# Kernel optimization log

Hardware: AMD Instinct MI355X
Metric: run time of the kernel (lower is better)

Reference implementation:

```python
import jax, jax.numpy as jnp
import numpy as np

N_NODES = 100000
N_EDGES = 1600000
IN_CH = 128
OUT_CH = 128


def setup_inputs() -> dict:
    key = jax.random.key(0)
    k1, k2, k3 = jax.random.split(key, 3)
    x = jax.random.normal(k1, (N_NODES, IN_CH), dtype=jnp.float32)
    edge_index = jax.random.randint(k2, (2, N_EDGES), 0, N_NODES, dtype=jnp.int64)
    # glorot-like init for the linear weight, stored as [in, out]
    W = jax.random.normal(k3, (IN_CH, OUT_CH), dtype=jnp.float32) * (2.0 / (IN_CH + OUT_CH)) ** 0.5
    bias = jnp.zeros((OUT_CH,), dtype=jnp.float32)
    return {"x": x, "edge_index": edge_index, "W": W, "bias": bias}


def reference(x, edge_index, W, bias):
    N = x.shape[0]
    # linear transform (bias-free, matches Linear(in, out, bias=False))
    h = x @ W  # [N, out]

    # add self loops (improved=False -> fill_value = 1.0)
    loop = jnp.arange(N, dtype=edge_index.dtype)
    src = jnp.concatenate([edge_index[0], loop])
    dst = jnp.concatenate([edge_index[1], loop])
    ew = jnp.ones(src.shape[0], dtype=h.dtype)  # edge_weight None -> ones

    # symmetric GCN normalization: deg from dst, norm = d^-1/2[src] * w * d^-1/2[dst]
    deg = jax.ops.segment_sum(ew, dst, num_segments=N)
    deg_inv_sqrt = jnp.where(deg > 0, jax.lax.rsqrt(deg), 0.0)
    w = deg_inv_sqrt[src] * ew * deg_inv_sqrt[dst]

    # spmm aggregation: out[dst] += w * h[src]
    out = jax.ops.segment_sum(h[src] * w[:, None], dst, num_segments=N)
    return out + bias
```

## Files before the change

kernel.cpp:

```cpp
#include <hip/hip_runtime.h>
#include <hip/hip_bf16.h>

constexpr int kNodes = 100000;
constexpr int kEdges = 1600000;
constexpr int kCh    = 128;
constexpr int kCap   = 32;
constexpr int kOvfCap = 4096;
constexpr int kLOvf  = 512;
constexpr int kBinShift = 8;
constexpr int kBinSize  = 1 << kBinShift;
constexpr int kBins  = (kNodes + kBinSize - 1) >> kBinShift;
constexpr int kABlocks = 128;
constexpr int kChunkCap = 64;
constexpr int kGemmBlocks = (kNodes + 127) / 128;
constexpr int kAggBlocks = (kNodes + 63) / 64;

typedef __attribute__((ext_vector_type(8))) short short8;
typedef __attribute__((ext_vector_type(4))) float floatx4;
typedef __attribute__((ext_vector_type(4))) int   intx4;


__global__ __launch_bounds__(512) void k_fused(const float* __restrict__ x,
                                               const float* __restrict__ W,
                                               const int* __restrict__ srcArr,
                                               const int* __restrict__ dstArr,
                                               unsigned* __restrict__ segs,
                                               int* __restrict__ segCnt,
                                               int* __restrict__ ovfCnt,
                                               int* __restrict__ ovfD,
                                               int* __restrict__ ovfS,
                                               __hip_bfloat16* __restrict__ hs) {
  if (blockIdx.x < kABlocks) {
    __shared__ int lcnt[kBins];
    for (int i = threadIdx.x; i < kBins; i += 512) lcnt[i] = 0;
    __syncthreads();
    const intx4* d4 = (const intx4*)dstArr;
    const intx4* s4 = (const intx4*)srcArr;
    unsigned* myseg = segs + (long)blockIdx.x * kBins * kChunkCap;
    for (int i = blockIdx.x * 512 + (int)threadIdx.x; i < kEdges / 4; i += kABlocks * 512) {
      intx4 dv = __builtin_nontemporal_load(d4 + i);
      intx4 sv = __builtin_nontemporal_load(s4 + i);
      #pragma unroll
      for (int k = 0; k < 4; k++) {
        int d = dv[k], s = sv[k];
        int bin = d >> kBinShift;
        int pos = atomicAdd(&lcnt[bin], 1);
        if (pos < kChunkCap) {
          myseg[bin * kChunkCap + pos] = ((unsigned)(d & (kBinSize - 1)) << 17) | (unsigned)s;
        } else {
          int o = atomicAdd(ovfCnt, 1);
          if (o < kOvfCap) { ovfD[o] = d; ovfS[o] = s; }
        }
      }
    }
    __syncthreads();
    for (int i = threadIdx.x; i < kBins; i += 512) {
      int c = lcnt[i];
      segCnt[blockIdx.x * kBins + i] = c < kChunkCap ? c : kChunkCap;
    }
    return;
  }

  __shared__ short8 Bf[2048];
  for (int e = threadIdx.x; e < 2048; e += 512) {
    int lane = e & 63, c = (e >> 6) & 3, tt = e >> 8;
    int quad = lane >> 4, mcol = lane & 15;
    short8 v;
    #pragma unroll
    for (int j = 0; j < 8; j++) {
      __hip_bfloat16 h = __float2bfloat16(W[(c * 32 + quad * 8 + j) * kCh + tt * 16 + mcol]);
      v[j] = *(short*)&h;
    }
    Bf[e] = v;
  }
  __syncthreads();

  int wave = threadIdx.x >> 6;
  int lane = threadIdx.x & 63;
  int quad = lane >> 4;
  int mcol = lane & 15;
  int gb = blockIdx.x - kABlocks;
  long rowBase = ((long)gb * 8 + wave) * 16;
  if (rowBase >= kNodes) return;

  long arow = rowBase + mcol;
  if (arow >= kNodes) arow = kNodes - 1;
  const float* xp = x + arow * kCh;
  short8 afrag[4];
  #pragma unroll
  for (int c = 0; c < 4; c++) {
    const floatx4* p = (const floatx4*)(xp + c * 32 + quad * 8);
    floatx4 v0 = __builtin_nontemporal_load(p);
    floatx4 v1 = __builtin_nontemporal_load(p + 1);
    #pragma unroll
    for (int j = 0; j < 4; j++) {
      __hip_bfloat16 h0 = __float2bfloat16(v0[j]);
      __hip_bfloat16 h1 = __float2bfloat16(v1[j]);
      afrag[c][j]     = *(short*)&h0;
      afrag[c][j + 4] = *(short*)&h1;
    }
  }

  #pragma unroll
  for (int t = 0; t < 8; t++) {
    floatx4 acc = {0.f, 0.f, 0.f, 0.f};
    #pragma unroll
    for (int c = 0; c < 4; c++) {
      short8 b = Bf[(t * 4 + c) * 64 + lane];
      acc = __builtin_amdgcn_mfma_f32_16x16x32_bf16(afrag[c], b, acc, 0, 0, 0);
    }
    #pragma unroll
    for (int i = 0; i < 4; i++) {
      long r = rowBase + quad * 4 + i;
      if (r < kNodes) {
        __hip_bfloat16 h = __float2bfloat16(acc[i]);
        __builtin_nontemporal_store(*(short*)&h, (short*)hs + r * kCh + t * 16 + mcol);
      }
    }
  }
}


__global__ __launch_bounds__(256) void k_dinv(const unsigned* __restrict__ segs,
                                              const int* __restrict__ segCnt,
                                              const int* __restrict__ ovfCnt,
                                              const int* __restrict__ ovfD,
                                              float* __restrict__ dinv) {
  __shared__ int lsn[kABlocks];
  __shared__ int hist[kBinSize];
  int bin = blockIdx.x;
  for (int i = threadIdx.x; i < kABlocks; i += 256) lsn[i] = segCnt[i * kBins + bin];
  for (int i = threadIdx.x; i < kBinSize; i += 256) hist[i] = 0;
  __syncthreads();

  for (int slot = threadIdx.x; slot < kABlocks * kChunkCap; slot += 256) {
    int blk = slot >> 6, pos = slot & (kChunkCap - 1);
    if (pos < lsn[blk]) {
      unsigned e = segs[((long)blk * kBins + bin) * kChunkCap + pos];
      atomicAdd(&hist[e >> 17], 1);
    }
  }
  int n = *ovfCnt; if (n > kOvfCap) n = kOvfCap;
  for (int i = threadIdx.x; i < n; i += 256) {
    int d = ovfD[i];
    if ((d >> kBinShift) == bin) atomicAdd(&hist[d & (kBinSize - 1)], 1);
  }
  __syncthreads();
  int base = bin << kBinShift;
  for (int i = threadIdx.x; i < kBinSize; i += 256) {
    int node = base + i;
    if (node < kNodes) dinv[node] = rsqrtf((float)(hist[i] + 1));
  }
}


__global__ __launch_bounds__(512) void k_agg(const unsigned* __restrict__ segs,
                                             const int* __restrict__ segCnt,
                                             const int* __restrict__ ovfCnt,
                                             const int* __restrict__ ovfD,
                                             const int* __restrict__ ovfS,
                                             const float* __restrict__ dinv,
                                             const __hip_bfloat16* __restrict__ hs,
                                             const float* __restrict__ bias,
                                             float* __restrict__ out) {
  __shared__ int lsn[kABlocks];
  __shared__ int lcnt[64];
  __shared__ __align__(16) int lbkt[64][kCap];
  __shared__ unsigned lovf[kLOvf];
  __shared__ int lovfn;

  int base = blockIdx.x * 64;
  int bin  = base >> kBinShift;
  int q    = (base >> 6) & 3;

  for (int i = threadIdx.x; i < kABlocks; i += 512) lsn[i] = segCnt[i * kBins + bin];
  for (int i = threadIdx.x; i < 64; i += 512) lcnt[i] = 0;
  if (threadIdx.x == 0) lovfn = 0;
  __syncthreads();

  for (int slot = threadIdx.x; slot < kABlocks * kChunkCap; slot += 512) {
    int blk = slot >> 6, pos = slot & (kChunkCap - 1);
    if (pos < lsn[blk]) {
      unsigned e = segs[((long)blk * kBins + bin) * kChunkCap + pos];
      int r = (int)(e >> 17) - q * 64;
      if ((unsigned)r < 64u) {
        int p = atomicAdd(&lcnt[r], 1);
        if (p < kCap) lbkt[r][p] = (int)(e & 0x1ffff);
        else { int o = atomicAdd(&lovfn, 1); if (o < kLOvf) lovf[o] = ((unsigned)r << 17) | (e & 0x1ffff); }
      }
    }
  }
  {
    int n = *ovfCnt; if (n > kOvfCap) n = kOvfCap;
    for (int i = threadIdx.x; i < n; i += 512) {
      int d = ovfD[i];
      if ((d >> 6) == blockIdx.x) {
        int r = d & 63;
        int p = atomicAdd(&lcnt[r], 1);
        if (p < kCap) lbkt[r][p] = ovfS[i];
        else { int o = atomicAdd(&lovfn, 1); if (o < kLOvf) lovf[o] = ((unsigned)r << 17) | (unsigned)ovfS[i]; }
      }
    }
  }
  __syncthreads();

  int wave = threadIdx.x >> 6;
  int lane = threadIdx.x & 63;
  const __hip_bfloat162* hbase = (const __hip_bfloat162*)hs;
  int novf = lovfn; if (novf > kLOvf) novf = kLOvf;

  for (int t = 0; t < 8; t++) {
    int r = wave * 8 + t;
    int node = base + r;
    if (node >= kNodes) break;

    float dd = dinv[node];
    float2 sf = __bfloat1622float2(hbase[(long)node * (kCh / 2) + lane]);
    float acc0 = dd * sf.x;
    float acc1 = dd * sf.y;

    int c = lcnt[r]; if (c > kCap) c = kCap;
    int j = 0;
    for (; j + 7 < c; j += 8) {
      int s[8];
      #pragma unroll
      for (int u = 0; u < 8; u++) s[u] = lbkt[r][j + u];
      float dv[8];
      #pragma unroll
      for (int u = 0; u < 8; u++) dv[u] = dinv[s[u]];
      __hip_bfloat162 v[8];
      #pragma unroll
      for (int u = 0; u < 8; u++) v[u] = hbase[(long)s[u] * (kCh / 2) + lane];
      #pragma unroll
      for (int u = 0; u < 8; u++) {
        float2 f = __bfloat1622float2(v[u]);
        acc0 = fmaf(dv[u], f.x, acc0);
        acc1 = fmaf(dv[u], f.y, acc1);
      }
    }
    for (; j < c; ++j) {
      int s = lbkt[r][j];
      float dv = dinv[s];
      float2 f = __bfloat1622float2(hbase[(long)s * (kCh / 2) + lane]);
      acc0 = fmaf(dv, f.x, acc0);
      acc1 = fmaf(dv, f.y, acc1);
    }
    for (int i = 0; i < novf; i++) {
      if ((int)(lovf[i] >> 17) == r) {
        int s = (int)(lovf[i] & 0x1ffff);
        float2 f = __bfloat1622float2(hbase[(long)s * (kCh / 2) + lane]);
        acc0 = fmaf(dinv[s], f.x, acc0);
        acc1 = fmaf(dinv[s], f.y, acc1);
      }
    }

    float2 b = ((const float2*)bias)[lane];
    float2 o;
    o.x = dd * acc0 + b.x;
    o.y = dd * acc1 + b.y;
    ((float2*)(out + (long)node * kCh))[lane] = o;
  }
}


extern "C" void kernel_launch(void* const* d_in, const int* in_sizes, int n_in,
                              void* d_out, int out_size, void* d_ws, size_t ws_size,
                              hipStream_t stream) {
  const float* x    = (const float*)d_in[0];
  const int*   ei   = (const int*)d_in[1];
  const float* W    = (const float*)d_in[2];
  const float* bias = (const float*)d_in[3];
  float* out = (float*)d_out;

  const int* srcArr = ei;
  const int* dstArr = ei + kEdges;

  char* ws = (char*)d_ws;
  size_t off = 0;
  __hip_bfloat16* hs = (__hip_bfloat16*)(ws + off); off += (size_t)kNodes * kCh * 2;
  unsigned* segs = (unsigned*)(ws + off); off += (size_t)kABlocks * kBins * kChunkCap * 4;
  float* dinv    = (float*)   (ws + off); off += (size_t)kNodes * 4;
  int*   segCnt  = (int*)     (ws + off); off += (size_t)kABlocks * kBins * 4;
  int*   ovfCnt  = (int*)     (ws + off); off += 64;
  int*   ovfD    = (int*)     (ws + off); off += (size_t)kOvfCap * 4;
  int*   ovfS    = (int*)     (ws + off); off += (size_t)kOvfCap * 4;

  (void)hipMemsetAsync(ovfCnt, 0, 64, stream);

  k_fused<<<kABlocks + kGemmBlocks, 512, 0, stream>>>(x, W, srcArr, dstArr,
                                                      segs, segCnt, ovfCnt, ovfD, ovfS, hs);

  k_dinv<<<kBins, 256, 0, stream>>>(segs, segCnt, ovfCnt, ovfD, dinv);

  k_agg<<<kAggBlocks, 512, 0, stream>>>(segs, segCnt, ovfCnt, ovfD, ovfS,
                                        dinv, hs, bias, out);
}
```

Baseline: 240.8 us.

## Shrink dst bins to 128 nodes and replace global overflow with per-block spill lists

Bins shrink from 256 to 128 nodes with 32-slot chunks per partition block. The aggregation kernel now handles a whole bin per block, so it no longer scans 256-node bins four times and discards three quarters of the entries. The global atomic overflow list and its memset are replaced by per-block shared-memory spill counters with small per-block spill arrays, and output stores become nontemporal. The risk is that the smaller chunk and spill capacities may silently drop edges on dense bins. With random dst indices, a partition block sees about 16 edges per bin, so 32 slots are usually enough.

```diff
diff --git a/kernel.cpp b/kernel.cpp
--- a/kernel.cpp
+++ b/kernel.cpp
@@ -5,19 +5,19 @@
 constexpr int kEdges = 1600000;
 constexpr int kCh    = 128;
 constexpr int kCap   = 32;
-constexpr int kOvfCap = 4096;
-constexpr int kLOvf  = 512;
-constexpr int kBinShift = 8;
+constexpr int kLOvf  = 256;
+constexpr int kBinShift = 7;
 constexpr int kBinSize  = 1 << kBinShift;
 constexpr int kBins  = (kNodes + kBinSize - 1) >> kBinShift;
 constexpr int kABlocks = 128;
-constexpr int kChunkCap = 64;
+constexpr int kChunkCap = 32;
+constexpr int kSpillCap = 64;
 constexpr int kGemmBlocks = (kNodes + 127) / 128;
-constexpr int kAggBlocks = (kNodes + 63) / 64;
 
 typedef __attribute__((ext_vector_type(8))) short short8;
 typedef __attribute__((ext_vector_type(4))) float floatx4;
 typedef __attribute__((ext_vector_type(4))) int   intx4;
+typedef __attribute__((ext_vector_type(2))) float floatx2;
 
 
 __global__ __launch_bounds__(512) void k_fused(const float* __restrict__ x,
@@ -26,13 +26,15 @@
                                                const int* __restrict__ dstArr,
                                                unsigned* __restrict__ segs,
                                                int* __restrict__ segCnt,
-                                               int* __restrict__ ovfCnt,
-                                               int* __restrict__ ovfD,
-                                               int* __restrict__ ovfS,
+                                               int* __restrict__ spillCnt,
+                                               int* __restrict__ spillD,
+                                               int* __restrict__ spillS,
                                                __hip_bfloat16* __restrict__ hs) {
   if (blockIdx.x < kABlocks) {
     __shared__ int lcnt[kBins];
+    __shared__ int lspilln;
     for (int i = threadIdx.x; i < kBins; i += 512) lcnt[i] = 0;
+    if (threadIdx.x == 0) lspilln = 0;
     __syncthreads();
     const intx4* d4 = (const intx4*)dstArr;
     const intx4* s4 = (const intx4*)srcArr;
@@ -46,10 +48,13 @@
         int bin = d >> kBinShift;
         int pos = atomicAdd(&lcnt[bin], 1);
         if (pos < kChunkCap) {
-          myseg[bin * kChunkCap + pos] = ((unsigned)(d & (kBinSize - 1)) << 17) | (unsigned)s;
+          myseg[(bin << 5) + pos] = ((unsigned)(d & (kBinSize - 1)) << 17) | (unsigned)s;
         } else {
-          int o = atomicAdd(ovfCnt, 1);
-          if (o < kOvfCap) { ovfD[o] = d; ovfS[o] = s; }
+          int o = atomicAdd(&lspilln, 1);
+          if (o < kSpillCap) {
+            spillD[blockIdx.x * kSpillCap + o] = d;
+            spillS[blockIdx.x * kSpillCap + o] = s;
+          }
         }
       }
     }
@@ -57,6 +62,10 @@
     for (int i = threadIdx.x; i < kBins; i += 512) {
       int c = lcnt[i];
       segCnt[blockIdx.x * kBins + i] = c < kChunkCap ? c : kChunkCap;
+    }
+    if (threadIdx.x == 0) {
+      int n = lspilln;
+      spillCnt[blockIdx.x] = n < kSpillCap ? n : kSpillCap;
     }
     return;
   }
@@ -123,27 +132,33 @@
 
 __global__ __launch_bounds__(256) void k_dinv(const unsigned* __restrict__ segs,
                                               const int* __restrict__ segCnt,
-                                              const int* __restrict__ ovfCnt,
-                                              const int* __restrict__ ovfD,
+                                              const int* __restrict__ spillCnt,
+                                              const int* __restrict__ spillD,
                                               float* __restrict__ dinv) {
   __shared__ int lsn[kABlocks];
+  __shared__ int lsp[kABlocks];
   __shared__ int hist[kBinSize];
   int bin = blockIdx.x;
-  for (int i = threadIdx.x; i < kABlocks; i += 256) lsn[i] = segCnt[i * kBins + bin];
+  for (int i = threadIdx.x; i < kABlocks; i += 256) {
+    lsn[i] = segCnt[i * kBins + bin];
+    lsp[i] = spillCnt[i];
+  }
   for (int i = threadIdx.x; i < kBinSize; i += 256) hist[i] = 0;
   __syncthreads();
 
   for (int slot = threadIdx.x; slot < kABlocks * kChunkCap; slot += 256) {
-    int blk = slot >> 6, pos = slot & (kChunkCap - 1);
+    int blk = slot >> 5, pos = slot & 31;
     if (pos < lsn[blk]) {
       unsigned e = segs[((long)blk * kBins + bin) * kChunkCap + pos];
       atomicAdd(&hist[e >> 17], 1);
     }
   }
-  int n = *ovfCnt; if (n > kOvfCap) n = kOvfCap;
-  for (int i = threadIdx.x; i < n; i += 256) {
-    int d = ovfD[i];
-    if ((d >> kBinShift) == bin) atomicAdd(&hist[d & (kBinSize - 1)], 1);
+  for (int i = threadIdx.x; i < kABlocks * kSpillCap; i += 256) {
+    int blk = i >> 6, o = i & 63;
+    if (o < lsp[blk]) {
+      int d = spillD[blk * kSpillCap + o];
+      if ((d >> kBinShift) == bin) atomicAdd(&hist[d & (kBinSize - 1)], 1);
+    }
   }
   __syncthreads();
   int base = bin << kBinShift;
@@ -156,49 +171,51 @@
 
 __global__ __launch_bounds__(512) void k_agg(const unsigned* __restrict__ segs,
                                              const int* __restrict__ segCnt,
-                                             const int* __restrict__ ovfCnt,
-                                             const int* __restrict__ ovfD,
-                                             const int* __restrict__ ovfS,
+                                             const int* __restrict__ spillCnt,
+                                             const int* __restrict__ spillD,
+                                             const int* __restrict__ spillS,
                                              const float* __restrict__ dinv,
                                              const __hip_bfloat16* __restrict__ hs,
                                              const float* __restrict__ bias,
                                              float* __restrict__ out) {
   __shared__ int lsn[kABlocks];
-  __shared__ int lcnt[64];
-  __shared__ __align__(16) int lbkt[64][kCap];
+  __shared__ int lsp[kABlocks];
+  __shared__ int lcnt[kBinSize];
+  __shared__ __align__(16) int lbkt[kBinSize][kCap];
   __shared__ unsigned lovf[kLOvf];
   __shared__ int lovfn;
 
-  int base = blockIdx.x * 64;
-  int bin  = base >> kBinShift;
-  int q    = (base >> 6) & 3;
-
-  for (int i = threadIdx.x; i < kABlocks; i += 512) lsn[i] = segCnt[i * kBins + bin];
-  for (int i = threadIdx.x; i < 64; i += 512) lcnt[i] = 0;
+  int bin  = blockIdx.x;
+  int base = bin << kBinShift;
+
+  for (int i = threadIdx.x; i < kABlocks; i += 512) {
+    lsn[i] = segCnt[i * kBins + bin];
+    lsp[i] = spillCnt[i];
+  }
+  for (int i = threadIdx.x; i < kBinSize; i += 512) lcnt[i] = 0;
   if (threadIdx.x == 0) lovfn = 0;
   __syncthreads();
 
   for (int slot = threadIdx.x; slot < kABlocks * kChunkCap; slot += 512) {
-    int blk = slot >> 6, pos = slot & (kChunkCap - 1);
+    int blk = slot >> 5, pos = slot & 31;
     if (pos < lsn[blk]) {
       unsigned e = segs[((long)blk * kBins + bin) * kChunkCap + pos];
-      int r = (int)(e >> 17) - q * 64;
-      if ((unsigned)r < 64u) {
+      int r = (int)(e >> 17);
+      int p = atomicAdd(&lcnt[r], 1);
+      if (p < kCap) lbkt[r][p] = (int)(e & 0x1ffff);
+      else { int o = atomicAdd(&lovfn, 1); if (o < kLOvf) lovf[o] = ((unsigned)r << 17) | (e & 0x1ffff); }
+    }
+  }
+  for (int i = threadIdx.x; i < kABlocks * kSpillCap; i += 512) {
+    int blk = i >> 6, o = i & 63;
+    if (o < lsp[blk]) {
+      int d = spillD[blk * kSpillCap + o];
+      if ((d >> kBinShift) == bin) {
+        int r = d & (kBinSize - 1);
+        int s = spillS[blk * kSpillCap + o];
         int p = atomicAdd(&lcnt[r], 1);
-        if (p < kCap) lbkt[r][p] = (int)(e & 0x1ffff);
-        else { int o = atomicAdd(&lovfn, 1); if (o < kLOvf) lovf[o] = ((unsigned)r << 17) | (e & 0x1ffff); }
-      }
-    }
-  }
-  {
-    int n = *ovfCnt; if (n > kOvfCap) n = kOvfCap;
-    for (int i = threadIdx.x; i < n; i += 512) {
-      int d = ovfD[i];
-      if ((d >> 6) == blockIdx.x) {
-        int r = d & 63;
-        int p = atomicAdd(&lcnt[r], 1);
-        if (p < kCap) lbkt[r][p] = ovfS[i];
-        else { int o = atomicAdd(&lovfn, 1); if (o < kLOvf) lovf[o] = ((unsigned)r << 17) | (unsigned)ovfS[i]; }
+        if (p < kCap) lbkt[r][p] = s;
+        else { int o2 = atomicAdd(&lovfn, 1); if (o2 < kLOvf) lovf[o2] = ((unsigned)r << 17) | (unsigned)s; }
       }
     }
   }
@@ -209,10 +226,10 @@
   const __hip_bfloat162* hbase = (const __hip_bfloat162*)hs;
   int novf = lovfn; if (novf > kLOvf) novf = kLOvf;
 
-  for (int t = 0; t < 8; t++) {
-    int r = wave * 8 + t;
+  for (int t = 0; t < 16; t++) {
+    int r = wave * 16 + t;
     int node = base + r;
-    if (node >= kNodes) break;
+    if (node >= kNodes) continue;
 
     float dd = dinv[node];
     float2 sf = __bfloat1622float2(hbase[(long)node * (kCh / 2) + lane]);
@@ -255,10 +272,10 @@
     }
 
     float2 b = ((const float2*)bias)[lane];
-    float2 o;
-    o.x = dd * acc0 + b.x;
-    o.y = dd * acc1 + b.y;
-    ((float2*)(out + (long)node * kCh))[lane] = o;
+    floatx2 o;
+    o[0] = dd * acc0 + b.x;
+    o[1] = dd * acc1 + b.y;
+    __builtin_nontemporal_store(o, (floatx2*)(out + (long)node * kCh) + lane);
   }
 }
 
@@ -281,17 +298,15 @@
   unsigned* segs = (unsigned*)(ws + off); off += (size_t)kABlocks * kBins * kChunkCap * 4;
   float* dinv    = (float*)   (ws + off); off += (size_t)kNodes * 4;
   int*   segCnt  = (int*)     (ws + off); off += (size_t)kABlocks * kBins * 4;
-  int*   ovfCnt  = (int*)     (ws + off); off += 64;
-  int*   ovfD    = (int*)     (ws + off); off += (size_t)kOvfCap * 4;
-  int*   ovfS    = (int*)     (ws + off); off += (size_t)kOvfCap * 4;
-
-  (void)hipMemsetAsync(ovfCnt, 0, 64, stream);
+  int*   spillCnt= (int*)     (ws + off); off += (size_t)kABlocks * 4;
+  int*   spillD  = (int*)     (ws + off); off += (size_t)kABlocks * kSpillCap * 4;
+  int*   spillS  = (int*)     (ws + off); off += (size_t)kABlocks * kSpillCap * 4;
 
   k_fused<<<kABlocks + kGemmBlocks, 512, 0, stream>>>(x, W, srcArr, dstArr,
-                                                      segs, segCnt, ovfCnt, ovfD, ovfS, hs);
-
-  k_dinv<<<kBins, 256, 0, stream>>>(segs, segCnt, ovfCnt, ovfD, dinv);
-
-  k_agg<<<kAggBlocks, 512, 0, stream>>>(segs, segCnt, ovfCnt, ovfD, ovfS,
-                                        dinv, hs, bias, out);
+                                                      segs, segCnt, spillCnt, spillD, spillS, hs);
+
+  k_dinv<<<kBins, 256, 0, stream>>>(segs, segCnt, spillCnt, spillD, dinv);
+
+  k_agg<<<kBins, 512, 0, stream>>>(segs, segCnt, spillCnt, spillD, spillS,
+                                   dinv, hs, bias, out);
 }
```

Result: faster. 233.8 us (-2.9%).
